# Kernel tuning notes

Hardware: AMD Instinct MI355X
Metric: run time of the kernel (lower is better)

The kernel has to match this reference:

```python
import jax, jax.numpy as jnp
import numpy as np

NUM_CENTROIDS = 8192
COMMITMENT = 0.25


def setup_inputs() -> dict:
    key = jax.random.key(0)
    k1, k2 = jax.random.split(key)
    B, T, D, K = 16, 2048, 512, NUM_CENTROIDS
    inputs = jax.random.normal(k1, (B, T, D), dtype=jnp.float32)
    # kaiming_normal_ on [K, D]: std = sqrt(2 / fan_in) with fan_in = D
    codebook = jax.random.normal(k2, (K, D), dtype=jnp.float32) * jnp.sqrt(2.0 / D)
    return {"inputs": inputs, "codebook": codebook, "train": 0}


def reference(inputs, codebook, train):
    D = inputs.shape[-1]
    K = codebook.shape[0]
    flat = inputs.reshape(-1, D)  # [N, D]

    distances = (
        jnp.sum(flat * flat, axis=1, keepdims=True)
        - 2.0 * (flat @ codebook.T)
        + jnp.sum(codebook * codebook, axis=1)[None, :]
    )
    nn_idx = jnp.argmin(distances, axis=1)  # [N]

    # one_hot @ codebook == gather (same math, no [N, K] one-hot materialized)
    quantized = codebook[nn_idx]  # [N, D]

    # VQ loss (codebook term) + commitment term
    quant_loss = jnp.square(quantized - jax.lax.stop_gradient(flat))
    quant_loss = quant_loss + COMMITMENT * jnp.square(
        jax.lax.stop_gradient(quantized) - flat
    )
    quantization_loss = quant_loss.reshape(inputs.shape)

    quantized = quantized.reshape(inputs.shape)
    # straight-through estimator
    quantized_out = inputs + jax.lax.stop_gradient(quantized - inputs)

    nn_idx = nn_idx.reshape(inputs.shape[:-1])[None, ...]  # [1, B, T]
    codebook_values = jax.lax.stop_gradient(codebook)[None, ...]  # [1, K, D]
    counts = jnp.ones((K,), dtype=jnp.float32)  # train=False: EMA counter untouched (init ones)

    return quantized_out, quantization_loss, nn_idx, codebook_values, counts
```

## Files before the change

### kernel.cpp

```cpp
#include <hip/hip_runtime.h>

#define NROWS 32768
#define DDIM  512
#define KCENT 8192

#define O_LOSS 16777216
#define O_IDX  33554432
#define O_CBV  33587200
#define O_CNT  37781504
#define O_PBLK 8388608

typedef float f32x4 __attribute__((ext_vector_type(4)));
typedef _Float16 f16x8 __attribute__((ext_vector_type(8)));

__global__ __launch_bounds__(256) void vq_cvt_swz8(
    const float* __restrict__ src, char* __restrict__ dst)
{
    const int gid = blockIdx.x * 256 + threadIdx.x;
    const int r = gid >> 6, w = gid & 63, dk = w >> 3, u = w & 7;
    const float4* p = (const float4*)(src + (size_t)r * DDIM + (dk*8 + (u ^ (r & 7))) * 8);
    float4 a = p[0], b = p[1];
    f16x8 h;
    h[0]=(_Float16)a.x; h[1]=(_Float16)a.y; h[2]=(_Float16)a.z; h[3]=(_Float16)a.w;
    h[4]=(_Float16)b.x; h[5]=(_Float16)b.y; h[6]=(_Float16)b.z; h[7]=(_Float16)b.w;
    *(f16x8*)(dst + (size_t)gid * 16) = h;
}

__global__ __launch_bounds__(256) void vq_cnorm_kernel(
    const float* __restrict__ CB, float* __restrict__ cnorm, float* __restrict__ counts)
{
    const int wid  = threadIdx.x >> 6;
    const int lane = threadIdx.x & 63;
    const int cid  = blockIdx.x * 4 + wid;
    const float4* p = (const float4*)(CB + (size_t)cid * DDIM + lane * 8);
    float4 a = p[0], b = p[1];
    double s = (double)a.x*a.x + (double)a.y*a.y + (double)a.z*a.z + (double)a.w*a.w
             + (double)b.x*b.x + (double)b.y*b.y + (double)b.z*b.z + (double)b.w*b.w;
    #pragma unroll
    for (int off = 32; off > 0; off >>= 1) s += __shfl_down(s, off);
    if (lane == 0) { cnorm[cid] = (float)s; counts[cid] = 1.0f; }
}

__device__ __forceinline__ void t2_update(float s, int c,
                                          float& v1, int& i1, float& v2, int& i2)
{
    if (s < v1)      { v2 = v1; i2 = i1; v1 = s; i1 = c; }
    else if (s < v2) { v2 = s;  i2 = c; }
}

__device__ __forceinline__ void t2_merge(float b1, int bi1, float b2, int bi2,
                                         float& a1, int& ai1, float& a2, int& ai2)
{
    if (b1 < a1 || (b1 == a1 && bi1 < ai1)) {
        float o1 = a1; int oi1 = ai1;
        a1 = b1; ai1 = bi1;
        if (b2 < o1 || (b2 == o1 && bi2 < oi1)) { a2 = b2; ai2 = bi2; }
        else                                    { a2 = o1; ai2 = oi1; }
    } else {
        if (b1 < a2 || (b1 == a2 && bi1 < ai2)) { a2 = b1; ai2 = bi1; }
    }
}

__device__ __forceinline__ void gl16(const char* g, const char* l)
{
    __builtin_amdgcn_global_load_lds(
        (const __attribute__((address_space(1))) void*)g,
        (__attribute__((address_space(3))) void*)l, 16, 0, 0);
}

__global__ __launch_bounds__(256, 4) void vq_gemm_kernel(
    const char* __restrict__ Xf, const char* __restrict__ Cf,
    const float* __restrict__ cnorm, float4* __restrict__ pblk)
{
    __shared__ __align__(16) char lds[32768];

    const int bid = blockIdx.x;
    const int xcd = bid & 7;
    const int idx = bid >> 3;
    const int cb  = xcd * 8 + (idx & 7);
    const int rb  = idx >> 3;

    const int t    = threadIdx.x;
    const int lane = t & 63;
    const int wid  = t >> 6;
    const int wr   = wid >> 1;
    const int wc   = wid & 1;
    const int l15  = lane & 15;
    const int lg   = lane >> 4;

    const size_t a0 = (size_t)(rb*128 + (t >> 3))*1024 + (t & 7)*16;
    const size_t b0 = (size_t)(cb*128 + (t >> 3))*1024 + (t & 7)*16;

    f32x4 acc[4][4];
    #pragma unroll
    for (int m = 0; m < 4; ++m)
        #pragma unroll
        for (int n = 0; n < 4; ++n) {
            f32x4 z = {0.f, 0.f, 0.f, 0.f};
            acc[m][n] = z;
        }

    for (int dk = 0; dk < 8; ++dk) {
        __syncthreads();
        #pragma unroll
        for (int i = 0; i < 4; ++i)
            gl16(Xf + a0 + i*32768 + dk*128, &lds[t*16 + i*4096]);
        #pragma unroll
        for (int i = 0; i < 4; ++i)
            gl16(Cf + b0 + i*32768 + dk*128, &lds[16384 + t*16 + i*4096]);
        __syncthreads();

        #pragma unroll
        for (int ks = 0; ks < 2; ++ks) {
            const int ku = ks*4 + lg;
            f16x8 A[4], B[4];
            #pragma unroll
            for (int m = 0; m < 4; ++m) {
                const int r = wr*64 + m*16 + l15;
                A[m] = *(const f16x8*)(&lds[r*128 + ((ku ^ (r & 7)) * 16)]);
            }
            #pragma unroll
            for (int n = 0; n < 4; ++n) {
                const int r = wc*64 + n*16 + l15;
                B[n] = *(const f16x8*)(&lds[16384 + r*128 + ((ku ^ (r & 7)) * 16)]);
            }
            #pragma unroll
            for (int m = 0; m < 4; ++m)
                #pragma unroll
                for (int n = 0; n < 4; ++n)
                    acc[m][n] = __builtin_amdgcn_mfma_f32_16x16x32_f16(A[m], B[n], acc[m][n], 0, 0, 0);
        }
    }
    __syncthreads();

    const int colbase = cb*128 + wc*64;
    float cn[4];
    int   cl[4];
    #pragma unroll
    for (int n = 0; n < 4; ++n) {
        cl[n] = colbase + n*16 + l15;
        cn[n] = cnorm[cl[n]];
    }
    float4* redq = (float4*)&lds[0];

    #pragma unroll
    for (int m = 0; m < 4; ++m)
        #pragma unroll
        for (int j = 0; j < 4; ++j) {
            float v1 = 3.4e38f, v2 = 3.4e38f;
            int   i1 = 0x7fffffff, i2 = 0x7fffffff;
            #pragma unroll
            for (int n = 0; n < 4; ++n)
                t2_update(fmaf(-2.0f, acc[m][n][j], cn[n]), cl[n], v1, i1, v2, i2);
            #pragma unroll
            for (int off = 1; off <= 8; off <<= 1) {
                float e1 = __shfl_xor(v1, off), e2 = __shfl_xor(v2, off);
                int  f1 = __shfl_xor(i1, off),  f2 = __shfl_xor(i2, off);
                t2_merge(e1, f1, e2, f2, v1, i1, v2, i2);
            }
            if (l15 == 0) {
                float4 w; w.x = v1; w.y = __int_as_float(i1);
                w.z = v2; w.w = __int_as_float(i2);
                redq[(wr*64 + m*16 + lg*4 + j)*2 + wc] = w;
            }
        }

    __syncthreads();
    if (t < 128) {
        float4 e0 = redq[t*2 + 0], e1 = redq[t*2 + 1];
        float v1 = e0.x, v2 = e0.z;
        int   i1 = __float_as_int(e0.y), i2 = __float_as_int(e0.w);
        t2_merge(e1.x, __float_as_int(e1.y), e1.z, __float_as_int(e1.w), v1, i1, v2, i2);
        float4 w; w.x = v1; w.y = __int_as_float(i1); w.z = v2; w.w = __int_as_float(i2);
        pblk[((size_t)(rb*128 + t))*64 + cb] = w;
    }
}

__global__ __launch_bounds__(256) void vq_merge_kernel(
    const float4* __restrict__ pblk, int* __restrict__ pmini2)
{
    const int wid  = threadIdx.x >> 6;
    const int lane = threadIdx.x & 63;
    const int row  = blockIdx.x * 4 + wid;
    float4 e = pblk[(size_t)row*64 + lane];
    float v1 = e.x, v2 = e.z;
    int   i1 = __float_as_int(e.y), i2 = __float_as_int(e.w);
    #pragma unroll
    for (int off = 1; off < 64; off <<= 1) {
        float b1 = __shfl_xor(v1, off), b2 = __shfl_xor(v2, off);
        int  c1 = __shfl_xor(i1, off),  c2 = __shfl_xor(i2, off);
        t2_merge(b1, c1, b2, c2, v1, i1, v2, i2);
    }
    if (lane == 0) { pmini2[row*2 + 0] = i1; pmini2[row*2 + 1] = i2; }
}

__global__ __launch_bounds__(256) void vq_resolve_out(
    const float* __restrict__ X, const float* __restrict__ CB,
    const int* __restrict__ pmini2, float* __restrict__ out)
{
    const int wid  = threadIdx.x >> 6;
    const int lane = threadIdx.x & 63;
    const int row  = blockIdx.x * 4 + wid;
    const int i0 = pmini2[row*2 + 0], i1 = pmini2[row*2 + 1];

    const float4* xp = (const float4*)(X + (size_t)row * DDIM + lane * 8);
    float4 xa = xp[0], xb = xp[1];
    const float4* p0 = (const float4*)(CB + (size_t)i0 * DDIM + lane * 8);
    float4 c0a = p0[0], c0b = p0[1];
    const float4* p1 = (const float4*)(CB + (size_t)i1 * DDIM + lane * 8);
    float4 c1a = p1[0], c1b = p1[1];

    double d0 = 0.0, d1 = 0.0, e;
    e = (double)xa.x - c0a.x; d0 += e*e;  e = (double)xa.y - c0a.y; d0 += e*e;
    e = (double)xa.z - c0a.z; d0 += e*e;  e = (double)xa.w - c0a.w; d0 += e*e;
    e = (double)xb.x - c0b.x; d0 += e*e;  e = (double)xb.y - c0b.y; d0 += e*e;
    e = (double)xb.z - c0b.z; d0 += e*e;  e = (double)xb.w - c0b.w; d0 += e*e;
    e = (double)xa.x - c1a.x; d1 += e*e;  e = (double)xa.y - c1a.y; d1 += e*e;
    e = (double)xa.z - c1a.z; d1 += e*e;  e = (double)xa.w - c1a.w; d1 += e*e;
    e = (double)xb.x - c1b.x; d1 += e*e;  e = (double)xb.y - c1b.y; d1 += e*e;
    e = (double)xb.z - c1b.z; d1 += e*e;  e = (double)xb.w - c1b.w; d1 += e*e;
    #pragma unroll
    for (int off = 1; off < 64; off <<= 1) {
        d0 += __shfl_xor(d0, off);
        d1 += __shfl_xor(d1, off);
    }

    const bool w1 = (d1 < d0) || (d1 == d0 && i1 < i0);
    const int idxw = w1 ? i1 : i0;
    float4 qa, qb;
    qa.x = w1 ? c1a.x : c0a.x;  qa.y = w1 ? c1a.y : c0a.y;
    qa.z = w1 ? c1a.z : c0a.z;  qa.w = w1 ? c1a.w : c0a.w;
    qb.x = w1 ? c1b.x : c0b.x;  qb.y = w1 ? c1b.y : c0b.y;
    qb.z = w1 ? c1b.z : c0b.z;  qb.w = w1 ? c1b.w : c0b.w;

    float4 qoa, loa, qob, lob;
    float d, s;
    d = qa.x - xa.x; qoa.x = xa.x + d; s = d*d; loa.x = s + 0.25f*s;
    d = qa.y - xa.y; qoa.y = xa.y + d; s = d*d; loa.y = s + 0.25f*s;
    d = qa.z - xa.z; qoa.z = xa.z + d; s = d*d; loa.z = s + 0.25f*s;
    d = qa.w - xa.w; qoa.w = xa.w + d; s = d*d; loa.w = s + 0.25f*s;
    d = qb.x - xb.x; qob.x = xb.x + d; s = d*d; lob.x = s + 0.25f*s;
    d = qb.y - xb.y; qob.y = xb.y + d; s = d*d; lob.y = s + 0.25f*s;
    d = qb.z - xb.z; qob.z = xb.z + d; s = d*d; lob.z = s + 0.25f*s;
    d = qb.w - xb.w; qob.w = xb.w + d; s = d*d; lob.w = s + 0.25f*s;

    ((float4*)out)[(size_t)row*128 + lane*2 + 0] = qoa;
    ((float4*)out)[(size_t)row*128 + lane*2 + 1] = qob;
    ((float4*)(out + O_LOSS))[(size_t)row*128 + lane*2 + 0] = loa;
    ((float4*)(out + O_LOSS))[(size_t)row*128 + lane*2 + 1] = lob;
    if (lane == 0) out[O_IDX + row] = (float)idxw;
}

extern "C" void kernel_launch(void* const* d_in, const int* in_sizes, int n_in,
                              void* d_out, int out_size, void* d_ws, size_t ws_size,
                              hipStream_t stream)
{
    const float* X  = (const float*)d_in[0];
    const float* CB = (const float*)d_in[1];
    float* out = (float*)d_out;

    char*   XsB  = (char*)out;
    float4* pblk = (float4*)(out + O_PBLK);
    char*   CBsB = (char*)(out + O_LOSS);

    float* cnorm  = (float*)d_ws;
    int*   pmini2 = (int*)(cnorm + KCENT);

    vq_cvt_swz8<<<(NROWS*64)/256, 256, 0, stream>>>(X, XsB);
    vq_cvt_swz8<<<(KCENT*64)/256, 256, 0, stream>>>(CB, CBsB);
    vq_cnorm_kernel<<<KCENT/4, 256, 0, stream>>>(CB, cnorm, out + O_CNT);
    vq_gemm_kernel<<<(NROWS/128)*(KCENT/128), 256, 0, stream>>>(XsB, CBsB, cnorm, pblk);
    vq_merge_kernel<<<NROWS/4, 256, 0, stream>>>(pblk, pmini2);
    vq_resolve_out<<<NROWS/4, 256, 0, stream>>>(X, CB, pmini2, out);
    hipMemcpyAsync(out + O_CBV, CB, (size_t)KCENT * DDIM * sizeof(float),
                   hipMemcpyDeviceToDevice, stream);
}
```

Baseline: 905.1 us.

## Restructure distance GEMM into row-resident sweep over codebook with double-buffered B

Replaces the 128x128 tiled GEMM with a kernel where each 512-thread block keeps a 64-row X tile (full D) resident in 128KB LDS and sweeps all 8192 centroids in 16 slabs of 512. Codebook chunks are double-buffered via async global-to-LDS loads with manual waitcnt/barriers, and top-2 reduction happens per slab, producing 16 partials per row instead of 64. The merge kernel becomes a per-thread 16-way serial merge. This cuts X reload traffic and partial-result volume, but uses 128KB LDS (one block per CU, low occupancy) and relies on hand-placed vmcnt barriers for correctness.

```diff
diff --git a/kernel.cpp b/kernel.cpp
--- a/kernel.cpp
+++ b/kernel.cpp
@@ -68,28 +68,39 @@
         (__attribute__((address_space(3))) void*)l, 16, 0, 0);
 }
 
-__global__ __launch_bounds__(256, 4) void vq_gemm_kernel(
+__global__ __launch_bounds__(512, 2) void vq_sweep_kernel(
     const char* __restrict__ Xf, const char* __restrict__ Cf,
     const float* __restrict__ cnorm, float4* __restrict__ pblk)
 {
-    __shared__ __align__(16) char lds[32768];
-
-    const int bid = blockIdx.x;
-    const int xcd = bid & 7;
-    const int idx = bid >> 3;
-    const int cb  = xcd * 8 + (idx & 7);
-    const int rb  = idx >> 3;
-
+    __shared__ __align__(16) char lds[131072];
+
+    const int blk  = blockIdx.x;
     const int t    = threadIdx.x;
     const int lane = t & 63;
-    const int wid  = t >> 6;
-    const int wr   = wid >> 1;
-    const int wc   = wid & 1;
+    const int cg   = t >> 6;
     const int l15  = lane & 15;
     const int lg   = lane >> 4;
 
-    const size_t a0 = (size_t)(rb*128 + (t >> 3))*1024 + (t & 7)*16;
-    const size_t b0 = (size_t)(cb*128 + (t >> 3))*1024 + (t & 7)*16;
+    #pragma unroll
+    for (int i = 0; i < 8; ++i) {
+        const int d = i*512 + t;
+        gl16(Xf + (size_t)(blk*64 + (d >> 6))*1024 + (d & 63)*16, &lds[d*16]);
+    }
+
+    #define STAGE_B(S, K, BUF) {                                              \
+        _Pragma("unroll")                                                     \
+        for (int i = 0; i < 4; ++i) {                                         \
+            const int d  = i*512 + t;                                         \
+            const int c  = d >> 2;                                            \
+            const int li = (d & 3) ^ ((c >> 1) & 3);                          \
+            const int sub = ((K) & 1)*4 + li;                                 \
+            gl16(Cf + (size_t)((S)*512 + c)*1024 + ((K) >> 1)*128             \
+                    + ((sub ^ (c & 7)) * 16),                                 \
+                 &lds[65536 + (BUF)*32768 + d*16]);                           \
+        } }
+
+    STAGE_B(0, 0, 0);
+    __syncthreads();
 
     f32x4 acc[4][4];
     #pragma unroll
@@ -100,98 +111,111 @@
             acc[m][n] = z;
         }
 
-    for (int dk = 0; dk < 8; ++dk) {
-        __syncthreads();
+    for (int s = 0; s < 16; ++s) {
         #pragma unroll
-        for (int i = 0; i < 4; ++i)
-            gl16(Xf + a0 + i*32768 + dk*128, &lds[t*16 + i*4096]);
-        #pragma unroll
-        for (int i = 0; i < 4; ++i)
-            gl16(Cf + b0 + i*32768 + dk*128, &lds[16384 + t*16 + i*4096]);
-        __syncthreads();
-
-        #pragma unroll
-        for (int ks = 0; ks < 2; ++ks) {
-            const int ku = ks*4 + lg;
+        for (int k = 0; k < 16; ++k) {
+            if (k < 15) {
+                STAGE_B(s, k + 1, (k + 1) & 1);
+                asm volatile("s_waitcnt vmcnt(4)\n\ts_barrier" ::: "memory");
+            } else if (s < 15) {
+                STAGE_B(s + 1, 0, 0);
+                asm volatile("s_waitcnt vmcnt(4)\n\ts_barrier" ::: "memory");
+            } else {
+                asm volatile("s_waitcnt vmcnt(0)\n\ts_barrier" ::: "memory");
+            }
+            const char* bb = &lds[65536 + (k & 1)*32768];
+            const int kb  = (k >> 1)*128;
+            const int sA  = (k & 1)*4 + lg;
             f16x8 A[4], B[4];
             #pragma unroll
             for (int m = 0; m < 4; ++m) {
-                const int r = wr*64 + m*16 + l15;
-                A[m] = *(const f16x8*)(&lds[r*128 + ((ku ^ (r & 7)) * 16)]);
+                const int r = m*16 + l15;
+                A[m] = *(const f16x8*)(&lds[r*1024 + kb + ((sA ^ (r & 7)) * 16)]);
             }
             #pragma unroll
             for (int n = 0; n < 4; ++n) {
-                const int r = wc*64 + n*16 + l15;
-                B[n] = *(const f16x8*)(&lds[16384 + r*128 + ((ku ^ (r & 7)) * 16)]);
+                const int c = cg*64 + n*16 + l15;
+                B[n] = *(const f16x8*)(bb + c*64 + ((lg ^ ((c >> 1) & 3)) * 16));
             }
             #pragma unroll
             for (int m = 0; m < 4; ++m)
                 #pragma unroll
                 for (int n = 0; n < 4; ++n)
                     acc[m][n] = __builtin_amdgcn_mfma_f32_16x16x32_f16(A[m], B[n], acc[m][n], 0, 0, 0);
+            asm volatile("s_barrier" ::: "memory");
         }
-    }
-    __syncthreads();
-
-    const int colbase = cb*128 + wc*64;
-    float cn[4];
-    int   cl[4];
-    #pragma unroll
-    for (int n = 0; n < 4; ++n) {
-        cl[n] = colbase + n*16 + l15;
-        cn[n] = cnorm[cl[n]];
-    }
-    float4* redq = (float4*)&lds[0];
-
-    #pragma unroll
-    for (int m = 0; m < 4; ++m)
-        #pragma unroll
-        for (int j = 0; j < 4; ++j) {
-            float v1 = 3.4e38f, v2 = 3.4e38f;
-            int   i1 = 0x7fffffff, i2 = 0x7fffffff;
-            #pragma unroll
-            for (int n = 0; n < 4; ++n)
-                t2_update(fmaf(-2.0f, acc[m][n][j], cn[n]), cl[n], v1, i1, v2, i2);
-            #pragma unroll
-            for (int off = 1; off <= 8; off <<= 1) {
-                float e1 = __shfl_xor(v1, off), e2 = __shfl_xor(v2, off);
-                int  f1 = __shfl_xor(i1, off),  f2 = __shfl_xor(i2, off);
-                t2_merge(e1, f1, e2, f2, v1, i1, v2, i2);
-            }
-            if (l15 == 0) {
-                float4 w; w.x = v1; w.y = __int_as_float(i1);
-                w.z = v2; w.w = __int_as_float(i2);
-                redq[(wr*64 + m*16 + lg*4 + j)*2 + wc] = w;
+
+        float4* red = (float4*)&lds[98304];
+        const int colb = s*512 + cg*64;
+        {
+            float cn[4];
+            #pragma unroll
+            for (int n = 0; n < 4; ++n) cn[n] = cnorm[colb + n*16 + l15];
+            #pragma unroll
+            for (int m = 0; m < 4; ++m) {
+                #pragma unroll
+                for (int j = 0; j < 4; ++j) {
+                    float v1 = 3.4e38f, v2 = 3.4e38f;
+                    int   i1 = 0x7fffffff, i2 = 0x7fffffff;
+                    #pragma unroll
+                    for (int n = 0; n < 4; ++n)
+                        t2_update(fmaf(-2.0f, acc[m][n][j], cn[n]),
+                                  colb + n*16 + l15, v1, i1, v2, i2);
+                    #pragma unroll
+                    for (int off = 1; off <= 8; off <<= 1) {
+                        float e1 = __shfl_xor(v1, off), e2 = __shfl_xor(v2, off);
+                        int  f1 = __shfl_xor(i1, off),  f2 = __shfl_xor(i2, off);
+                        t2_merge(e1, f1, e2, f2, v1, i1, v2, i2);
+                    }
+                    if (l15 == 0) {
+                        float4 w; w.x = v1; w.y = __int_as_float(i1);
+                        w.z = v2; w.w = __int_as_float(i2);
+                        red[(m*16 + lg*4 + j)*8 + cg] = w;
+                    }
+                }
+                #pragma unroll
+                for (int n = 0; n < 4; ++n) {
+                    f32x4 z = {0.f, 0.f, 0.f, 0.f};
+                    acc[m][n] = z;
+                }
             }
         }
-
-    __syncthreads();
-    if (t < 128) {
-        float4 e0 = redq[t*2 + 0], e1 = redq[t*2 + 1];
-        float v1 = e0.x, v2 = e0.z;
-        int   i1 = __float_as_int(e0.y), i2 = __float_as_int(e0.w);
-        t2_merge(e1.x, __float_as_int(e1.y), e1.z, __float_as_int(e1.w), v1, i1, v2, i2);
-        float4 w; w.x = v1; w.y = __int_as_float(i1); w.z = v2; w.w = __int_as_float(i2);
-        pblk[((size_t)(rb*128 + t))*64 + cb] = w;
-    }
-}
-
-__global__ __launch_bounds__(256) void vq_merge_kernel(
+        asm volatile("s_waitcnt lgkmcnt(0)\n\ts_barrier" ::: "memory");
+        if (t < 64) {
+            float4 e0 = red[t*8 + 0];
+            float v1 = e0.x, v2 = e0.z;
+            int   i1 = __float_as_int(e0.y), i2 = __float_as_int(e0.w);
+            #pragma unroll
+            for (int w8 = 1; w8 < 8; ++w8) {
+                float4 e = red[t*8 + w8];
+                t2_merge(e.x, __float_as_int(e.y), e.z, __float_as_int(e.w),
+                         v1, i1, v2, i2);
+            }
+            float4 w; w.x = v1; w.y = __int_as_float(i1);
+            w.z = v2; w.w = __int_as_float(i2);
+            pblk[(size_t)(blk*64 + t)*16 + s] = w;
+        }
+        asm volatile("s_waitcnt lgkmcnt(0)\n\ts_barrier" ::: "memory");
+    }
+    #undef STAGE_B
+}
+
+__global__ __launch_bounds__(256) void vq_merge16(
     const float4* __restrict__ pblk, int* __restrict__ pmini2)
 {
-    const int wid  = threadIdx.x >> 6;
-    const int lane = threadIdx.x & 63;
-    const int row  = blockIdx.x * 4 + wid;
-    float4 e = pblk[(size_t)row*64 + lane];
-    float v1 = e.x, v2 = e.z;
-    int   i1 = __float_as_int(e.y), i2 = __float_as_int(e.w);
-    #pragma unroll
-    for (int off = 1; off < 64; off <<= 1) {
-        float b1 = __shfl_xor(v1, off), b2 = __shfl_xor(v2, off);
-        int  c1 = __shfl_xor(i1, off),  c2 = __shfl_xor(i2, off);
-        t2_merge(b1, c1, b2, c2, v1, i1, v2, i2);
-    }
-    if (lane == 0) { pmini2[row*2 + 0] = i1; pmini2[row*2 + 1] = i2; }
+    const int row = blockIdx.x * 256 + threadIdx.x;
+    const float4* e = pblk + (size_t)row * 16;
+    float4 e0 = e[0];
+    float v1 = e0.x, v2 = e0.z;
+    int   i1 = __float_as_int(e0.y), i2 = __float_as_int(e0.w);
+    #pragma unroll
+    for (int s = 1; s < 16; ++s) {
+        float4 es = e[s];
+        t2_merge(es.x, __float_as_int(es.y), es.z, __float_as_int(es.w),
+                 v1, i1, v2, i2);
+    }
+    pmini2[row*2 + 0] = i1;
+    pmini2[row*2 + 1] = i2;
 }
 
 __global__ __launch_bounds__(256) void vq_resolve_out(
@@ -269,8 +293,8 @@
     vq_cvt_swz8<<<(NROWS*64)/256, 256, 0, stream>>>(X, XsB);
     vq_cvt_swz8<<<(KCENT*64)/256, 256, 0, stream>>>(CB, CBsB);
     vq_cnorm_kernel<<<KCENT/4, 256, 0, stream>>>(CB, cnorm, out + O_CNT);
-    vq_gemm_kernel<<<(NROWS/128)*(KCENT/128), 256, 0, stream>>>(XsB, CBsB, cnorm, pblk);
-    vq_merge_kernel<<<NROWS/4, 256, 0, stream>>>(pblk, pmini2);
+    vq_sweep_kernel<<<NROWS/64, 512, 0, stream>>>(XsB, CBsB, cnorm, pblk);
+    vq_merge16<<<NROWS/256, 256, 0, stream>>>(pblk, pmini2);
     vq_resolve_out<<<NROWS/4, 256, 0, stream>>>(X, CB, pmini2, out);
     hipMemcpyAsync(out + O_CBV, CB, (size_t)KCENT * DDIM * sizeof(float),
                    hipMemcpyDeviceToDevice, stream);
```

New measurement: 1.339 ms. +48.0%, slower.

## Enlarge GEMM tile to 256x256 with 16 waves and double-buffered LDS prefetch

Applied to the files above, without the earlier changes.

The distance GEMM now uses 1024-thread blocks covering 256x256 output tiles instead of 256x128-row tiles. The next K-slice is prefetched into a second LDS buffer via global_load_lds while MFMAs run on the current one, synchronised with explicit vmcnt waits and barriers. With half as many column blocks, the merge kernel becomes a per-thread serial reduction over 32 partials. The aim is more operand reuse per load and hidden global latency. The cost is 128 KB of LDS per block, which limits occupancy to one block per CU, and a launch_bounds minimum of 4 that cannot be met with 1024 threads.

```diff
diff --git a/kernel.cpp b/kernel.cpp
--- a/kernel.cpp
+++ b/kernel.cpp
@@ -68,28 +68,34 @@
         (__attribute__((address_space(3))) void*)l, 16, 0, 0);
 }
 
-__global__ __launch_bounds__(256, 4) void vq_gemm_kernel(
+__global__ __launch_bounds__(1024, 4) void vq_gemm_kernel(
     const char* __restrict__ Xf, const char* __restrict__ Cf,
     const float* __restrict__ cnorm, float4* __restrict__ pblk)
 {
-    __shared__ __align__(16) char lds[32768];
+    __shared__ __align__(16) char lds[131072];
 
     const int bid = blockIdx.x;
     const int xcd = bid & 7;
     const int idx = bid >> 3;
-    const int cb  = xcd * 8 + (idx & 7);
-    const int rb  = idx >> 3;
+    const int cb  = xcd * 4 + (idx & 3);
+    const int rb  = idx >> 2;
 
     const int t    = threadIdx.x;
     const int lane = t & 63;
     const int wid  = t >> 6;
-    const int wr   = wid >> 1;
-    const int wc   = wid & 1;
+    const int wr   = wid >> 2;
+    const int wc   = wid & 3;
     const int l15  = lane & 15;
     const int lg   = lane >> 4;
 
-    const size_t a0 = (size_t)(rb*128 + (t >> 3))*1024 + (t & 7)*16;
-    const size_t b0 = (size_t)(cb*128 + (t >> 3))*1024 + (t & 7)*16;
+    const size_t a0 = (size_t)(rb*256 + (t >> 3))*1024 + (t & 7)*16;
+    const size_t b0 = (size_t)(cb*256 + (t >> 3))*1024 + (t & 7)*16;
+
+    #define STAGE(dk, buf) {                                             \
+        gl16(Xf + a0          + (dk)*128, &lds[(buf)*65536 +         t*16]); \
+        gl16(Xf + a0 + 131072 + (dk)*128, &lds[(buf)*65536 + 16384 + t*16]); \
+        gl16(Cf + b0          + (dk)*128, &lds[(buf)*65536 + 32768 + t*16]); \
+        gl16(Cf + b0 + 131072 + (dk)*128, &lds[(buf)*65536 + 49152 + t*16]); }
 
     f32x4 acc[4][4];
     #pragma unroll
@@ -100,16 +106,17 @@
             acc[m][n] = z;
         }
 
+    STAGE(0, 0);
+    __syncthreads();
+
     for (int dk = 0; dk < 8; ++dk) {
-        __syncthreads();
-        #pragma unroll
-        for (int i = 0; i < 4; ++i)
-            gl16(Xf + a0 + i*32768 + dk*128, &lds[t*16 + i*4096]);
-        #pragma unroll
-        for (int i = 0; i < 4; ++i)
-            gl16(Cf + b0 + i*32768 + dk*128, &lds[16384 + t*16 + i*4096]);
-        __syncthreads();
-
+        if (dk < 7) {
+            STAGE(dk + 1, (dk + 1) & 1);
+            asm volatile("s_waitcnt vmcnt(4)\n\ts_barrier" ::: "memory");
+        } else {
+            asm volatile("s_waitcnt vmcnt(0)\n\ts_barrier" ::: "memory");
+        }
+        const char* bb = &lds[(dk & 1)*65536];
         #pragma unroll
         for (int ks = 0; ks < 2; ++ks) {
             const int ku = ks*4 + lg;
@@ -117,12 +124,12 @@
             #pragma unroll
             for (int m = 0; m < 4; ++m) {
                 const int r = wr*64 + m*16 + l15;
-                A[m] = *(const f16x8*)(&lds[r*128 + ((ku ^ (r & 7)) * 16)]);
+                A[m] = *(const f16x8*)(bb + r*128 + ((ku ^ (r & 7)) * 16));
             }
             #pragma unroll
             for (int n = 0; n < 4; ++n) {
                 const int r = wc*64 + n*16 + l15;
-                B[n] = *(const f16x8*)(&lds[16384 + r*128 + ((ku ^ (r & 7)) * 16)]);
+                B[n] = *(const f16x8*)(bb + 32768 + r*128 + ((ku ^ (r & 7)) * 16));
             }
             #pragma unroll
             for (int m = 0; m < 4; ++m)
@@ -130,10 +137,11 @@
                 for (int n = 0; n < 4; ++n)
                     acc[m][n] = __builtin_amdgcn_mfma_f32_16x16x32_f16(A[m], B[n], acc[m][n], 0, 0, 0);
         }
-    }
-    __syncthreads();
-
-    const int colbase = cb*128 + wc*64;
+        asm volatile("s_barrier" ::: "memory");
+    }
+    #undef STAGE
+
+    const int colbase = cb*256 + wc*64;
     float cn[4];
     int   cl[4];
     #pragma unroll
@@ -161,37 +169,40 @@
             if (l15 == 0) {
                 float4 w; w.x = v1; w.y = __int_as_float(i1);
                 w.z = v2; w.w = __int_as_float(i2);
-                redq[(wr*64 + m*16 + lg*4 + j)*2 + wc] = w;
+                redq[(wr*64 + m*16 + lg*4 + j)*4 + wc] = w;
             }
         }
 
     __syncthreads();
-    if (t < 128) {
-        float4 e0 = redq[t*2 + 0], e1 = redq[t*2 + 1];
+    if (t < 256) {
+        float4 e0 = redq[t*4 + 0], e1 = redq[t*4 + 1];
+        float4 e2 = redq[t*4 + 2], e3 = redq[t*4 + 3];
         float v1 = e0.x, v2 = e0.z;
         int   i1 = __float_as_int(e0.y), i2 = __float_as_int(e0.w);
         t2_merge(e1.x, __float_as_int(e1.y), e1.z, __float_as_int(e1.w), v1, i1, v2, i2);
+        t2_merge(e2.x, __float_as_int(e2.y), e2.z, __float_as_int(e2.w), v1, i1, v2, i2);
+        t2_merge(e3.x, __float_as_int(e3.y), e3.z, __float_as_int(e3.w), v1, i1, v2, i2);
         float4 w; w.x = v1; w.y = __int_as_float(i1); w.z = v2; w.w = __int_as_float(i2);
-        pblk[((size_t)(rb*128 + t))*64 + cb] = w;
-    }
-}
-
-__global__ __launch_bounds__(256) void vq_merge_kernel(
+        pblk[((size_t)(rb*256 + t))*32 + cb] = w;
+    }
+}
+
+__global__ __launch_bounds__(256) void vq_merge32(
     const float4* __restrict__ pblk, int* __restrict__ pmini2)
 {
-    const int wid  = threadIdx.x >> 6;
-    const int lane = threadIdx.x & 63;
-    const int row  = blockIdx.x * 4 + wid;
-    float4 e = pblk[(size_t)row*64 + lane];
-    float v1 = e.x, v2 = e.z;
-    int   i1 = __float_as_int(e.y), i2 = __float_as_int(e.w);
-    #pragma unroll
-    for (int off = 1; off < 64; off <<= 1) {
-        float b1 = __shfl_xor(v1, off), b2 = __shfl_xor(v2, off);
-        int  c1 = __shfl_xor(i1, off),  c2 = __shfl_xor(i2, off);
-        t2_merge(b1, c1, b2, c2, v1, i1, v2, i2);
-    }
-    if (lane == 0) { pmini2[row*2 + 0] = i1; pmini2[row*2 + 1] = i2; }
+    const int row = blockIdx.x * 256 + threadIdx.x;
+    const float4* e = pblk + (size_t)row * 32;
+    float4 e0 = e[0];
+    float v1 = e0.x, v2 = e0.z;
+    int   i1 = __float_as_int(e0.y), i2 = __float_as_int(e0.w);
+    #pragma unroll
+    for (int s = 1; s < 32; ++s) {
+        float4 es = e[s];
+        t2_merge(es.x, __float_as_int(es.y), es.z, __float_as_int(es.w),
+                 v1, i1, v2, i2);
+    }
+    pmini2[row*2 + 0] = i1;
+    pmini2[row*2 + 1] = i2;
 }
 
 __global__ __launch_bounds__(256) void vq_resolve_out(
@@ -269,8 +280,8 @@
     vq_cvt_swz8<<<(NROWS*64)/256, 256, 0, stream>>>(X, XsB);
     vq_cvt_swz8<<<(KCENT*64)/256, 256, 0, stream>>>(CB, CBsB);
     vq_cnorm_kernel<<<KCENT/4, 256, 0, stream>>>(CB, cnorm, out + O_CNT);
-    vq_gemm_kernel<<<(NROWS/128)*(KCENT/128), 256, 0, stream>>>(XsB, CBsB, cnorm, pblk);
-    vq_merge_kernel<<<NROWS/4, 256, 0, stream>>>(pblk, pmini2);
+    vq_gemm_kernel<<<(NROWS/256)*(KCENT/256), 1024, 0, stream>>>(XsB, CBsB, cnorm, pblk);
+    vq_merge32<<<NROWS/256, 256, 0, stream>>>(pblk, pmini2);
     vq_resolve_out<<<NROWS/4, 256, 0, stream>>>(X, CB, pmini2, out);
     hipMemcpyAsync(out + O_CBV, CB, (size_t)KCENT * DDIM * sizeof(float),
                    hipMemcpyDeviceToDevice, stream);
```

Result: slower. 964.9 us (+6.6%).
